# Performance work log

Measured on AMD Instinct MI355X. Metric: run time of the kernel, lower is better.

## Reference

```python
import jax, jax.numpy as jnp
import numpy as np

B, N, D, F, NDRV, PASSES = 64, 50000, 16, 5, 1000, 4


def setup_inputs() -> dict:
    key = jax.random.key(0)
    ks = jax.random.split(key, 12)
    inp = {
        "x": jax.random.normal(ks[0], (B, N), jnp.float32),
        "neighbor_idx": jax.random.randint(ks[1], (N, D), 0, N),
        "driver_idx": jnp.sort(jax.random.randint(ks[2], (NDRV,), 0, N)),
    }
    # conv stack: 1->5, five of 5->5, 5->1 (kernel [1,3])
    chans = [(1, F)] + [(F, F)] * 5 + [(F, 1)]
    for i, (ci, co) in enumerate(chans):
        inp[f"w{i}"] = jax.random.normal(ks[3 + i], (co, ci, 1, 3), jnp.float32) * 0.1
        inp[f"b{i}"] = jnp.zeros((co,), jnp.float32)
    return inp


def _conv1x3(z, w, b):
    # z: [B,C,N,W], w: [O,C,1,3] -> [B,O,N,W-2]
    out = jax.lax.conv_general_dilated(
        z, w, window_strides=(1, 1), padding='VALID',
        dimension_numbers=('NCHW', 'OIHW', 'NCHW'))
    return out + b[None, :, None, None]


def reference(x, neighbor_idx, driver_idx,
              w0, b0, w1, b1, w2, b2, w3, b3, w4, b4, w5, b5, w6, b6):
    params = [(w0, b0), (w1, b1), (w2, b2), (w3, b3), (w4, b4), (w5, b5), (w6, b6)]
    z = x  # [B, N]
    for _ in range(PASSES):
        g = z[:, neighbor_idx]            # neighbor gather -> [B, N, D]
        h = g[:, None]                    # [B, 1, N, D]  (input_preprocessor output)
        for w, b in params:
            h = jax.nn.relu(_conv1x3(h, w, b))  # relu after every conv (all but pool)
        h = 0.5 * (h[..., :-1] + h[..., 1:])    # AvgPool [1,2] stride 1: width 2 -> 1
        z = h.reshape(x.shape[0], -1)           # [B, N] (single channel, width 1)
    # final: mean over singleton channel dim then driver gather == direct gather
    return z[:, driver_idx]                      # [B, NDRV]
```

## Files before the change

### kernel.cpp

```cpp
#include <hip/hip_runtime.h>

#define NB    50000
#define BB    64
#define DD    16
#define NDRVN 1000

__device__ __forceinline__ float vg(float s) {
    asm("" : "+v"(s));
    return s;
}

__global__ __launch_bounds__(256) void transpose_kernel(
    const float* __restrict__ x, float* __restrict__ xT)
{
    int tid = blockIdx.x * 256 + threadIdx.x;
    int n = tid >> 6;
    int b = tid & 63;
    if (n < NB) xT[tid] = x[b * NB + n];
}

template<int WOUT>
__device__ __forceinline__ void conv5(const float (&in)[5][14], float (&out)[5][14],
                                      const float* __restrict__ w,
                                      const float* __restrict__ bias)
{
#pragma unroll
    for (int c = 0; c < 5; ++c) {
        float wr[15];
#pragma unroll
        for (int t = 0; t < 15; ++t) wr[t] = vg(w[c * 15 + t]);
        float bc = vg(bias[c]);
#pragma unroll
        for (int x = 0; x < WOUT; ++x) {
            float acc = bc;
#pragma unroll
            for (int ci = 0; ci < 5; ++ci) {
                acc = fmaf(wr[ci * 3 + 0], in[ci][x + 0], acc);
                acc = fmaf(wr[ci * 3 + 1], in[ci][x + 1], acc);
                acc = fmaf(wr[ci * 3 + 2], in[ci][x + 2], acc);
            }
            out[c][x] = fmaxf(acc, 0.0f);
        }
    }
}

__global__ __launch_bounds__(256)
__attribute__((amdgpu_waves_per_eu(2, 8)))
void pass_kernel(
    const float* __restrict__ zin, float* __restrict__ zout,
    const int*  __restrict__ nidx,
    const float* __restrict__ w0, const float* __restrict__ b0,
    const float* __restrict__ w1, const float* __restrict__ b1,
    const float* __restrict__ w2, const float* __restrict__ b2,
    const float* __restrict__ w3, const float* __restrict__ b3,
    const float* __restrict__ w4, const float* __restrict__ b4,
    const float* __restrict__ w5, const float* __restrict__ b5,
    const float* __restrict__ w6, const float* __restrict__ b6)
{
    int tid  = blockIdx.x * 256 + threadIdx.x;
    int lane = tid & 63;
    int n = __builtin_amdgcn_readfirstlane(tid >> 6);

    const int* ip = nidx + n * DD;

    float g[16];
#pragma unroll
    for (int d = 0; d < 16; ++d) {
        int j = ip[d];
        g[d] = zin[(size_t)j * BB + lane];
    }

    float ha[5][14], hb[5][14];

#pragma unroll
    for (int c = 0; c < 5; ++c) {
        float wa = vg(w0[c * 3 + 0]), wb = vg(w0[c * 3 + 1]), wc = vg(w0[c * 3 + 2]);
        float bc = vg(b0[c]);
#pragma unroll
        for (int x = 0; x < 14; ++x) {
            float acc = bc;
            acc = fmaf(wa, g[x + 0], acc);
            acc = fmaf(wb, g[x + 1], acc);
            acc = fmaf(wc, g[x + 2], acc);
            ha[c][x] = fmaxf(acc, 0.0f);
        }
    }

    conv5<12>(ha, hb, w1, b1);
    conv5<10>(hb, ha, w2, b2);
    conv5<8> (ha, hb, w3, b3);
    conv5<6> (hb, ha, w4, b4);
    conv5<4> (ha, hb, w5, b5);

    float bias6 = vg(b6[0]);
    float t0 = bias6, t1 = bias6;
#pragma unroll
    for (int ci = 0; ci < 5; ++ci) {
        float wa = vg(w6[ci * 3 + 0]), wb = vg(w6[ci * 3 + 1]), wc = vg(w6[ci * 3 + 2]);
        t0 = fmaf(wa, hb[ci][0], t0);
        t0 = fmaf(wb, hb[ci][1], t0);
        t0 = fmaf(wc, hb[ci][2], t0);
        t1 = fmaf(wa, hb[ci][1], t1);
        t1 = fmaf(wb, hb[ci][2], t1);
        t1 = fmaf(wc, hb[ci][3], t1);
    }
    t0 = fmaxf(t0, 0.0f);
    t1 = fmaxf(t1, 0.0f);

    zout[(size_t)n * BB + lane] = 0.5f * (t0 + t1);
}

__global__ __launch_bounds__(256) void gather_out_kernel(
    const float* __restrict__ z, const int* __restrict__ didx,
    float* __restrict__ out)
{
    int i = blockIdx.x * 256 + threadIdx.x;
    if (i >= BB * NDRVN) return;
    int b = i / NDRVN;
    int k = i - b * NDRVN;
    out[i] = z[(size_t)didx[k] * BB + b];
}

extern "C" void kernel_launch(void* const* d_in, const int* in_sizes, int n_in,
                              void* d_out, int out_size, void* d_ws, size_t ws_size,
                              hipStream_t stream)
{
    const float* x    = (const float*)d_in[0];
    const int*   nidx = (const int*)  d_in[1];
    const int*   didx = (const int*)  d_in[2];
    const float* w[7];
    const float* b[7];
    for (int i = 0; i < 7; ++i) {
        w[i] = (const float*)d_in[3 + 2 * i];
        b[i] = (const float*)d_in[4 + 2 * i];
    }

    float* z0 = (float*)d_ws;
    float* z1 = z0 + (size_t)NB * BB;

    const int blocks = (NB * BB) / 256;

    transpose_kernel<<<blocks, 256, 0, stream>>>(x, z0);

    pass_kernel<<<blocks, 256, 0, stream>>>(z0, z1, nidx,
        w[0], b[0], w[1], b[1], w[2], b[2], w[3], b[3],
        w[4], b[4], w[5], b[5], w[6], b[6]);
    pass_kernel<<<blocks, 256, 0, stream>>>(z1, z0, nidx,
        w[0], b[0], w[1], b[1], w[2], b[2], w[3], b[3],
        w[4], b[4], w[5], b[5], w[6], b[6]);
    pass_kernel<<<blocks, 256, 0, stream>>>(z0, z1, nidx,
        w[0], b[0], w[1], b[1], w[2], b[2], w[3], b[3],
        w[4], b[4], w[5], b[5], w[6], b[6]);
    pass_kernel<<<blocks, 256, 0, stream>>>(z1, z0, nidx,
        w[0], b[0], w[1], b[1], w[2], b[2], w[3], b[3],
        w[4], b[4], w[5], b[5], w[6], b[6]);

    gather_out_kernel<<<(BB * NDRVN + 255) / 256, 256, 0, stream>>>(z0, didx, (float*)d_out);
}
```

Before: 900.1 us.

## Process two nodes per wave using packed f2 FMA in pass kernel

```diff
diff --git a/kernel.cpp b/kernel.cpp
--- a/kernel.cpp
+++ b/kernel.cpp
@@ -5,9 +5,22 @@
 #define DD    16
 #define NDRVN 1000
 
+typedef float f2 __attribute__((ext_vector_type(2)));
+
 __device__ __forceinline__ float vg(float s) {
     asm("" : "+v"(s));
     return s;
+}
+
+__device__ __forceinline__ f2 pf(f2 a, f2 b, f2 c) {
+    return __builtin_elementwise_fma(a, b, c);
+}
+__device__ __forceinline__ f2 relu2(f2 a) {
+    return __builtin_elementwise_max(a, (f2)0.0f);
+}
+__device__ __forceinline__ f2 splat(float s) {
+    float v = vg(s);
+    return (f2){v, v};
 }
 
 __global__ __launch_bounds__(256) void transpose_kernel(
@@ -19,27 +32,31 @@
     if (n < NB) xT[tid] = x[b * NB + n];
 }
 
-template<int WOUT>
-__device__ __forceinline__ void conv5(const float (&in)[5][14], float (&out)[5][14],
-                                      const float* __restrict__ w,
-                                      const float* __restrict__ bias)
+template<int WIN>
+__device__ __forceinline__ void conv5p(const f2 (&in)[5][14], f2 (&out)[5][14],
+                                       const float* __restrict__ w,
+                                       const float* __restrict__ bias)
 {
+    constexpr int WOUT = WIN - 2;
+    f2 wr[75];
 #pragma unroll
-    for (int c = 0; c < 5; ++c) {
-        float wr[15];
+    for (int t = 0; t < 75; ++t) wr[t] = splat(w[t]);
+    f2 bb[5];
 #pragma unroll
-        for (int t = 0; t < 15; ++t) wr[t] = vg(w[c * 15 + t]);
-        float bc = vg(bias[c]);
+    for (int c = 0; c < 5; ++c) bb[c] = splat(bias[c]);
+
 #pragma unroll
-        for (int x = 0; x < WOUT; ++x) {
-            float acc = bc;
+    for (int x = 0; x < WOUT; ++x) {
+#pragma unroll
+        for (int c = 0; c < 5; ++c) {
+            f2 acc = bb[c];
 #pragma unroll
             for (int ci = 0; ci < 5; ++ci) {
-                acc = fmaf(wr[ci * 3 + 0], in[ci][x + 0], acc);
-                acc = fmaf(wr[ci * 3 + 1], in[ci][x + 1], acc);
-                acc = fmaf(wr[ci * 3 + 2], in[ci][x + 2], acc);
+                acc = pf(wr[c * 15 + ci * 3 + 0], in[ci][x + 0], acc);
+                acc = pf(wr[c * 15 + ci * 3 + 1], in[ci][x + 1], acc);
+                acc = pf(wr[c * 15 + ci * 3 + 2], in[ci][x + 2], acc);
             }
-            out[c][x] = fmaxf(acc, 0.0f);
+            out[c][x] = relu2(acc);
         }
     }
 }
@@ -57,57 +74,70 @@
     const float* __restrict__ w5, const float* __restrict__ b5,
     const float* __restrict__ w6, const float* __restrict__ b6)
 {
-    int tid  = blockIdx.x * 256 + threadIdx.x;
-    int lane = tid & 63;
-    int n = __builtin_amdgcn_readfirstlane(tid >> 6);
+    int lane   = threadIdx.x & 63;
+    int waveid = blockIdx.x * 4 + (threadIdx.x >> 6);
+    int n0 = __builtin_amdgcn_readfirstlane(waveid * 2);
 
-    const int* ip = nidx + n * DD;
+    const int* ip = nidx + n0 * DD;
 
-    float g[16];
+    f2 g[16];
 #pragma unroll
     for (int d = 0; d < 16; ++d) {
-        int j = ip[d];
-        g[d] = zin[(size_t)j * BB + lane];
+        float a = zin[(size_t)ip[d]      * BB + lane];
+        float b = zin[(size_t)ip[16 + d] * BB + lane];
+        g[d] = (f2){a, b};
     }
 
-    float ha[5][14], hb[5][14];
+    f2 ha[5][14], hb[5][14];
 
+    {
+        f2 wr[15], bb[5];
 #pragma unroll
-    for (int c = 0; c < 5; ++c) {
-        float wa = vg(w0[c * 3 + 0]), wb = vg(w0[c * 3 + 1]), wc = vg(w0[c * 3 + 2]);
-        float bc = vg(b0[c]);
+        for (int t = 0; t < 15; ++t) wr[t] = splat(w0[t]);
+#pragma unroll
+        for (int c = 0; c < 5; ++c) bb[c] = splat(b0[c]);
 #pragma unroll
         for (int x = 0; x < 14; ++x) {
-            float acc = bc;
-            acc = fmaf(wa, g[x + 0], acc);
-            acc = fmaf(wb, g[x + 1], acc);
-            acc = fmaf(wc, g[x + 2], acc);
-            ha[c][x] = fmaxf(acc, 0.0f);
+#pragma unroll
+            for (int c = 0; c < 5; ++c) {
+                f2 acc = bb[c];
+                acc = pf(wr[c * 3 + 0], g[x + 0], acc);
+                acc = pf(wr[c * 3 + 1], g[x + 1], acc);
+                acc = pf(wr[c * 3 + 2], g[x + 2], acc);
+                ha[c][x] = relu2(acc);
+            }
         }
     }
 
-    conv5<12>(ha, hb, w1, b1);
-    conv5<10>(hb, ha, w2, b2);
-    conv5<8> (ha, hb, w3, b3);
-    conv5<6> (hb, ha, w4, b4);
-    conv5<4> (ha, hb, w5, b5);
+    conv5p<14>(ha, hb, w1, b1);
+    conv5p<12>(hb, ha, w2, b2);
+    conv5p<10>(ha, hb, w3, b3);
+    conv5p<8> (hb, ha, w4, b4);
+    conv5p<6> (ha, hb, w5, b5);
 
-    float bias6 = vg(b6[0]);
-    float t0 = bias6, t1 = bias6;
+    {
+        f2 wr[15];
 #pragma unroll
-    for (int ci = 0; ci < 5; ++ci) {
-        float wa = vg(w6[ci * 3 + 0]), wb = vg(w6[ci * 3 + 1]), wc = vg(w6[ci * 3 + 2]);
-        t0 = fmaf(wa, hb[ci][0], t0);
-        t0 = fmaf(wb, hb[ci][1], t0);
-        t0 = fmaf(wc, hb[ci][2], t0);
-        t1 = fmaf(wa, hb[ci][1], t1);
-        t1 = fmaf(wb, hb[ci][2], t1);
-        t1 = fmaf(wc, hb[ci][3], t1);
+        for (int t = 0; t < 15; ++t) wr[t] = splat(w6[t]);
+        f2 bias = splat(b6[0]);
+        f2 t0 = bias, t1 = bias;
+#pragma unroll
+        for (int ci = 0; ci < 5; ++ci) {
+            t0 = pf(wr[ci * 3 + 0], hb[ci][0], t0);
+            t0 = pf(wr[ci * 3 + 1], hb[ci][1], t0);
+            t0 = pf(wr[ci * 3 + 2], hb[ci][2], t0);
+            t1 = pf(wr[ci * 3 + 0], hb[ci][1], t1);
+            t1 = pf(wr[ci * 3 + 1], hb[ci][2], t1);
+            t1 = pf(wr[ci * 3 + 2], hb[ci][3], t1);
+        }
+        t0 = relu2(t0);
+        t1 = relu2(t1);
+        f2 o;
+        o.x = 0.5f * (t0.x + t1.x);
+        o.y = 0.5f * (t0.y + t1.y);
+        zout[(size_t)n0 * BB + lane]       = o.x;
+        zout[(size_t)(n0 + 1) * BB + lane] = o.y;
     }
-    t0 = fmaxf(t0, 0.0f);
-    t1 = fmaxf(t1, 0.0f);
-
-    zout[(size_t)n * BB + lane] = 0.5f * (t0 + t1);
 }
 
 __global__ __launch_bounds__(256) void gather_out_kernel(
@@ -138,20 +168,21 @@
     float* z0 = (float*)d_ws;
     float* z1 = z0 + (size_t)NB * BB;
 
-    const int blocks = (NB * BB) / 256;
+    const int tblocks = (NB * BB) / 256;
+    const int pblocks = NB / 8;
 
-    transpose_kernel<<<blocks, 256, 0, stream>>>(x, z0);
+    transpose_kernel<<<tblocks, 256, 0, stream>>>(x, z0);
 
-    pass_kernel<<<blocks, 256, 0, stream>>>(z0, z1, nidx,
+    pass_kernel<<<pblocks, 256, 0, stream>>>(z0, z1, nidx,
         w[0], b[0], w[1], b[1], w[2], b[2], w[3], b[3],
         w[4], b[4], w[5], b[5], w[6], b[6]);
-    pass_kernel<<<blocks, 256, 0, stream>>>(z1, z0, nidx,
+    pass_kernel<<<pblocks, 256, 0, stream>>>(z1, z0, nidx,
         w[0], b[0], w[1], b[1], w[2], b[2], w[3], b[3],
         w[4], b[4], w[5], b[5], w[6], b[6]);
-    pass_kernel<<<blocks, 256, 0, stream>>>(z0, z1, nidx,
+    pass_kernel<<<pblocks, 256, 0, stream>>>(z0, z1, nidx,
         w[0], b[0], w[1], b[1], w[2], b[2], w[3], b[3],
         w[4], b[4], w[5], b[5], w[6], b[6]);
-    pass_kernel<<<blocks, 256, 0, stream>>>(z1, z0, nidx,
+    pass_kernel<<<pblocks, 256, 0, stream>>>(z1, z0, nidx,
         w[0], b[0], w[1], b[1], w[2], b[2], w[3], b[3],
         w[4], b[4], w[5], b[5], w[6], b[6]);
 
```

New measurement: 896.3 us. About the same (-0.4%).
